# Kernel tuning notes

Measured on AMD Instinct MI355X. Metric: run time of the kernel, lower is better.

The kernel has to match this reference:

```python
import jax, jax.numpy as jnp
import numpy as np

NUM_ITEMS = 100000
OUT_DIM = 128
BATCH = 16384
HIST = 50
TOTAL = BATCH * HIST


def setup_inputs() -> dict:
    key = jax.random.key(0)
    k1, k2, k3, k4, k5, k6 = jax.random.split(key, 6)
    feature_ids = jax.random.randint(k1, (TOTAL,), 0, NUM_ITEMS + 1, dtype=jnp.int64 if jax.config.jax_enable_x64 else jnp.int32)
    # ratings in {0.5, 1.0, ..., 5.0} so that (r - 0.5) * 2 is an int index in [0, 10)
    ratings = jax.random.randint(k2, (TOTAL,), 0, 10).astype(jnp.float32) / 2.0 + 0.5
    segment_ids = jnp.repeat(jnp.arange(BATCH, dtype=jnp.int32), HIST)  # [TOTAL]
    item_ids = jax.random.randint(k3, (BATCH,), 0, NUM_ITEMS, dtype=jnp.int32)
    # kaiming_uniform_(a=sqrt(5)) on an [N, D] table -> U(-b, b) with b = sqrt(6 / ((1 + 5) * D)) = 1/sqrt(D)
    b = 1.0 / np.sqrt(OUT_DIM)
    user_W = jax.random.uniform(k4, (NUM_ITEMS + 1, OUT_DIM), jnp.float32, -b, b)
    rating_W = jax.random.uniform(k5, (10, OUT_DIM), jnp.float32, -b, b)
    item_W = jax.random.uniform(k6, (NUM_ITEMS, OUT_DIM), jnp.float32, -b, b)
    bias = jnp.zeros((OUT_DIM,), jnp.float32)
    return {"feature_ids": feature_ids, "ratings": ratings, "segment_ids": segment_ids,
            "item_ids": item_ids, "user_W": user_W, "rating_W": rating_W,
            "item_W": item_W, "bias": bias}


def reference(feature_ids, ratings, segment_ids, item_ids, user_W, rating_W, item_W, bias):
    batch = item_ids.shape[0]
    rating_idx = ((ratings - 0.5) * 2.0).astype(jnp.int32)          # [T], in [0, 10)
    rating_weights = rating_W[rating_idx]                            # [T, D] gather
    user_weights = user_W[feature_ids] * rating_weights              # [T, D] gather + multiply
    user_sum = jax.ops.segment_sum(user_weights, segment_ids, num_segments=batch)  # [B, D]
    return user_sum + item_W[item_ids] + bias                        # [B, D]
```

## Files before the change

### kernel.cpp

```cpp
#include <hip/hip_runtime.h>


#define BATCH     16384
#define HIST      50
#define TOTAL     (BATCH * HIST)
#define UNROLL    10
#define DIM4      32
#define NROWS_U   100001
#define SLICES    4
#define SL_U4     (NROWS_U * 4)
#define UT_BYTES  ((size_t)SLICES * SL_U4 * 16)
#define RPB       64
#define BLOCK     256
#define RWPAD     36

typedef unsigned int u32x4 __attribute__((ext_vector_type(4)));

__global__ __launch_bounds__(256) void convert_pack_kernel(
    const float4* __restrict__ src,
    const int*    __restrict__ feature_ids,
    const float*  __restrict__ ratings,
    u32x4*        __restrict__ uT,
    int*          __restrict__ packed)
{
    const int tid = blockIdx.x * 256 + threadIdx.x;
    const int stride = gridDim.x * 256;
    if (blockIdx.y < SLICES) {
        const int slice = blockIdx.y;
        u32x4* dst = uT + (size_t)slice * SL_U4;
        for (int i = tid; i < SL_U4; i += stride) {
            const int row = i >> 2, q = i & 3;
            const float4 a = src[row * DIM4 + slice * 8 + q * 2];
            const float4 b = src[row * DIM4 + slice * 8 + q * 2 + 1];
            union { u32x4 v; _Float16 h[8]; } o;
            o.h[0] = (_Float16)a.x; o.h[1] = (_Float16)a.y;
            o.h[2] = (_Float16)a.z; o.h[3] = (_Float16)a.w;
            o.h[4] = (_Float16)b.x; o.h[5] = (_Float16)b.y;
            o.h[6] = (_Float16)b.z; o.h[7] = (_Float16)b.w;
            dst[i] = o.v;
        }
    } else {
        for (int t = tid; t < TOTAL; t += stride) {
            const int fid  = feature_ids[t];
            const int ridx = (int)(ratings[t] * 2.0f) - 1;
            packed[t] = (fid << 4) | ridx;
        }
    }
}

__global__ __launch_bounds__(BLOCK, 4) void features_linear_sliced(
    const int*    __restrict__ packed,
    const int*    __restrict__ item_ids,
    const u32x4*  __restrict__ uT,
    const float*  __restrict__ rating_Wf,
    const float4* __restrict__ item_W,
    const float4* __restrict__ bias,
    float4*       __restrict__ out)
{
    __shared__ int   sh_pid[RPB * HIST];
    __shared__ float sh_rW[10 * RWPAD];

    const int tid   = threadIdx.x;
    const int slice = blockIdx.x & 3;
    const int grp   = blockIdx.x >> 2;

    for (int i = tid; i < 10 * 32; i += BLOCK) {
        const int r = i >> 5, j = i & 31;
        sh_rW[r * RWPAD + j] = rating_Wf[r * 128 + slice * 32 + j];
    }

    const int base = grp * (RPB * HIST);
    for (int i = tid; i < RPB * HIST; i += BLOCK)
        sh_pid[i] = packed[base + i];
    __syncthreads();

    const int row = tid >> 2;
    const int q   = tid & 3;
    const int b   = grp * RPB + row;
    const int off = row * HIST;

    const u32x4* us = uT + (size_t)slice * SL_U4;

    float a0 = 0.f, a1 = 0.f, a2 = 0.f, a3 = 0.f,
          a4 = 0.f, a5 = 0.f, a6 = 0.f, a7 = 0.f;

    for (int h = 0; h < HIST; h += UNROLL) {
        const int p0 = sh_pid[off + h + 0], p1 = sh_pid[off + h + 1];
        const int p2 = sh_pid[off + h + 2], p3 = sh_pid[off + h + 3];
        const int p4 = sh_pid[off + h + 4], p5 = sh_pid[off + h + 5];
        const int p6 = sh_pid[off + h + 6], p7 = sh_pid[off + h + 7];
        const int p8 = sh_pid[off + h + 8], p9 = sh_pid[off + h + 9];

        u32x4 u0 = us[(p0 >> 4) * 4 + q];
        u32x4 u1 = us[(p1 >> 4) * 4 + q];
        u32x4 u2 = us[(p2 >> 4) * 4 + q];
        u32x4 u3 = us[(p3 >> 4) * 4 + q];
        u32x4 u4 = us[(p4 >> 4) * 4 + q];
        u32x4 u5 = us[(p5 >> 4) * 4 + q];
        u32x4 u6 = us[(p6 >> 4) * 4 + q];
        u32x4 u7 = us[(p7 >> 4) * 4 + q];
        u32x4 u8 = us[(p8 >> 4) * 4 + q];
        u32x4 u9 = us[(p9 >> 4) * 4 + q];

        asm volatile("" : "+v"(u0), "+v"(u1), "+v"(u2), "+v"(u3), "+v"(u4),
                          "+v"(u5), "+v"(u6), "+v"(u7), "+v"(u8), "+v"(u9));

#define CONSUME(uk, pk)                                                  \
        {                                                                \
            union { u32x4 v; _Float16 hh[8]; } c; c.v = uk;              \
            const float* w = &sh_rW[(pk & 15) * RWPAD + q * 8];          \
            a0 += (float)c.hh[0] * w[0]; a1 += (float)c.hh[1] * w[1];    \
            a2 += (float)c.hh[2] * w[2]; a3 += (float)c.hh[3] * w[3];    \
            a4 += (float)c.hh[4] * w[4]; a5 += (float)c.hh[5] * w[5];    \
            a6 += (float)c.hh[6] * w[6]; a7 += (float)c.hh[7] * w[7];    \
        }
        CONSUME(u0, p0) CONSUME(u1, p1) CONSUME(u2, p2) CONSUME(u3, p3)
        CONSUME(u4, p4) CONSUME(u5, p5) CONSUME(u6, p6) CONSUME(u7, p7)
        CONSUME(u8, p8) CONSUME(u9, p9)
#undef CONSUME
    }

    const int    iid = item_ids[b];
    const int    e   = slice * 8 + q * 2;
    const float4 iw0 = item_W[iid * DIM4 + e];
    const float4 iw1 = item_W[iid * DIM4 + e + 1];
    const float4 bs0 = bias[e];
    const float4 bs1 = bias[e + 1];

    float4 o0, o1;
    o0.x = a0 + iw0.x + bs0.x; o0.y = a1 + iw0.y + bs0.y;
    o0.z = a2 + iw0.z + bs0.z; o0.w = a3 + iw0.w + bs0.w;
    o1.x = a4 + iw1.x + bs1.x; o1.y = a5 + iw1.y + bs1.y;
    o1.z = a6 + iw1.z + bs1.z; o1.w = a7 + iw1.w + bs1.w;
    out[b * DIM4 + e]     = o0;
    out[b * DIM4 + e + 1] = o1;
}

__global__ __launch_bounds__(BLOCK) void features_linear_f32(
    const int*    __restrict__ feature_ids,
    const float*  __restrict__ ratings,
    const int*    __restrict__ item_ids,
    const float4* __restrict__ user_W,
    const float4* __restrict__ rating_W,
    const float4* __restrict__ item_W,
    const float4* __restrict__ bias,
    float4*       __restrict__ out)
{
    __shared__ float4 sh_rW[10 * DIM4];
    __shared__ int    sh_fid[8 * HIST];
    __shared__ int    sh_ridx[8 * HIST];

    const int tid = threadIdx.x;
    for (int i = tid; i < 10 * DIM4; i += BLOCK) sh_rW[i] = rating_W[i];
    const int base = blockIdx.x * (8 * HIST);
    for (int i = tid; i < 8 * HIST; i += BLOCK) {
        sh_fid[i] = feature_ids[base + i];
        float r = ratings[base + i];
        sh_ridx[i] = (int)(r * 2.0f) - 1;
    }
    __syncthreads();

    const int row = tid >> 5;
    const int d4  = tid & 31;
    const int b   = blockIdx.x * 8 + row;

    float4 acc; acc.x = 0.f; acc.y = 0.f; acc.z = 0.f; acc.w = 0.f;
    const int off = row * HIST;

    for (int h = 0; h < HIST; h += UNROLL) {
        int f[UNROLL], r[UNROLL];
#pragma unroll
        for (int i = 0; i < UNROLL; ++i) {
            f[i] = sh_fid[off + h + i];
            r[i] = sh_ridx[off + h + i];
        }
        float4 u[UNROLL];
#pragma unroll
        for (int i = 0; i < UNROLL; ++i) u[i] = user_W[f[i] * DIM4 + d4];
#pragma unroll
        for (int i = 0; i < UNROLL; ++i) {
            const float4 w = sh_rW[r[i] * DIM4 + d4];
            acc.x += u[i].x * w.x;
            acc.y += u[i].y * w.y;
            acc.z += u[i].z * w.z;
            acc.w += u[i].w * w.w;
        }
    }

    const int    iid = item_ids[b];
    const float4 iw  = item_W[iid * DIM4 + d4];
    const float4 bs  = bias[d4];

    float4 o;
    o.x = acc.x + iw.x + bs.x;
    o.y = acc.y + iw.y + bs.y;
    o.z = acc.z + iw.z + bs.z;
    o.w = acc.w + iw.w + bs.w;
    out[b * DIM4 + d4] = o;
}

extern "C" void kernel_launch(void* const* d_in, const int* in_sizes, int n_in,
                              void* d_out, int out_size, void* d_ws, size_t ws_size,
                              hipStream_t stream) {
    const int*    feature_ids = (const int*)   d_in[0];
    const float*  ratings     = (const float*) d_in[1];
    const int*    item_ids    = (const int*)   d_in[3];
    const float4* user_W      = (const float4*)d_in[4];
    const float4* rating_W    = (const float4*)d_in[5];
    const float4* item_W      = (const float4*)d_in[6];
    const float4* bias        = (const float4*)d_in[7];
    float4*       out         = (float4*)      d_out;

    const size_t need = UT_BYTES + (size_t)TOTAL * sizeof(int);
    if (d_ws != nullptr && ws_size >= need) {
        u32x4* uT     = (u32x4*)d_ws;
        int*   packed = (int*)((char*)d_ws + UT_BYTES);

        convert_pack_kernel<<<dim3(784, 5), dim3(256), 0, stream>>>(
            user_W, feature_ids, ratings, uT, packed);

        features_linear_sliced<<<dim3((BATCH / RPB) * SLICES), dim3(BLOCK), 0, stream>>>(
            packed, item_ids, uT, (const float*)rating_W, item_W, bias, out);
    } else {
        features_linear_f32<<<dim3(BATCH / 8), dim3(BLOCK), 0, stream>>>(
            feature_ids, ratings, item_ids, user_W, rating_W, item_W, bias, out);
    }
}
```

Measured before the change: 167.9 us.

## Split history across half-blocks with shared reduction and coalesce table conversion

The sliced gather kernel now handles 32 rows per block, with two groups of 64 threads each summing half of the 50-entry history for the same rows. The partial sums are then combined through shared memory, and launch bounds are raised to allow 8 blocks per SM for more memory-level parallelism. The fp16 conversion kernel now reads the source table linearly, scatters into the sliced layout, and uses a different grid shape. The cost is an extra barrier and reduction, a lower unroll depth per thread, and scattered writes during conversion.

```diff
diff --git a/kernel.cpp b/kernel.cpp
--- a/kernel.cpp
+++ b/kernel.cpp
@@ -4,13 +4,13 @@
 #define BATCH     16384
 #define HIST      50
 #define TOTAL     (BATCH * HIST)
-#define UNROLL    10
+#define UNROLL    5
 #define DIM4      32
 #define NROWS_U   100001
 #define SLICES    4
 #define SL_U4     (NROWS_U * 4)
 #define UT_BYTES  ((size_t)SLICES * SL_U4 * 16)
-#define RPB       64
+#define RPB       32
 #define BLOCK     256
 #define RWPAD     36
 
@@ -25,19 +25,17 @@
 {
     const int tid = blockIdx.x * 256 + threadIdx.x;
     const int stride = gridDim.x * 256;
-    if (blockIdx.y < SLICES) {
-        const int slice = blockIdx.y;
-        u32x4* dst = uT + (size_t)slice * SL_U4;
-        for (int i = tid; i < SL_U4; i += stride) {
-            const int row = i >> 2, q = i & 3;
-            const float4 a = src[row * DIM4 + slice * 8 + q * 2];
-            const float4 b = src[row * DIM4 + slice * 8 + q * 2 + 1];
+    if (blockIdx.y == 0) {
+        for (int n = tid; n < NROWS_U * 16; n += stride) {
+            const int row = n >> 4, s = (n >> 2) & 3, q = n & 3;
+            const float4 a = src[2 * n];
+            const float4 b = src[2 * n + 1];
             union { u32x4 v; _Float16 h[8]; } o;
             o.h[0] = (_Float16)a.x; o.h[1] = (_Float16)a.y;
             o.h[2] = (_Float16)a.z; o.h[3] = (_Float16)a.w;
             o.h[4] = (_Float16)b.x; o.h[5] = (_Float16)b.y;
             o.h[6] = (_Float16)b.z; o.h[7] = (_Float16)b.w;
-            dst[i] = o.v;
+            uT[(size_t)s * SL_U4 + row * 4 + q] = o.v;
         }
     } else {
         for (int t = tid; t < TOTAL; t += stride) {
@@ -48,7 +46,7 @@
     }
 }
 
-__global__ __launch_bounds__(BLOCK, 4) void features_linear_sliced(
+__global__ __launch_bounds__(BLOCK, 8) void features_linear_sliced(
     const int*    __restrict__ packed,
     const int*    __restrict__ item_ids,
     const u32x4*  __restrict__ uT,
@@ -59,6 +57,7 @@
 {
     __shared__ int   sh_pid[RPB * HIST];
     __shared__ float sh_rW[10 * RWPAD];
+    __shared__ float sh_red[128][8];
 
     const int tid   = threadIdx.x;
     const int slice = blockIdx.x & 3;
@@ -68,72 +67,76 @@
         const int r = i >> 5, j = i & 31;
         sh_rW[r * RWPAD + j] = rating_Wf[r * 128 + slice * 32 + j];
     }
-
     const int base = grp * (RPB * HIST);
     for (int i = tid; i < RPB * HIST; i += BLOCK)
         sh_pid[i] = packed[base + i];
     __syncthreads();
 
-    const int row = tid >> 2;
-    const int q   = tid & 3;
-    const int b   = grp * RPB + row;
-    const int off = row * HIST;
+    const int quad = tid >> 2;
+    const int q    = tid & 3;
+    const int row  = quad & 31;
+    const int hh   = quad >> 5;
+    const int off  = row * HIST + hh * 25;
 
     const u32x4* us = uT + (size_t)slice * SL_U4;
 
     float a0 = 0.f, a1 = 0.f, a2 = 0.f, a3 = 0.f,
           a4 = 0.f, a5 = 0.f, a6 = 0.f, a7 = 0.f;
 
-    for (int h = 0; h < HIST; h += UNROLL) {
+    for (int h = 0; h < 25; h += UNROLL) {
         const int p0 = sh_pid[off + h + 0], p1 = sh_pid[off + h + 1];
         const int p2 = sh_pid[off + h + 2], p3 = sh_pid[off + h + 3];
-        const int p4 = sh_pid[off + h + 4], p5 = sh_pid[off + h + 5];
-        const int p6 = sh_pid[off + h + 6], p7 = sh_pid[off + h + 7];
-        const int p8 = sh_pid[off + h + 8], p9 = sh_pid[off + h + 9];
+        const int p4 = sh_pid[off + h + 4];
 
         u32x4 u0 = us[(p0 >> 4) * 4 + q];
         u32x4 u1 = us[(p1 >> 4) * 4 + q];
         u32x4 u2 = us[(p2 >> 4) * 4 + q];
         u32x4 u3 = us[(p3 >> 4) * 4 + q];
         u32x4 u4 = us[(p4 >> 4) * 4 + q];
-        u32x4 u5 = us[(p5 >> 4) * 4 + q];
-        u32x4 u6 = us[(p6 >> 4) * 4 + q];
-        u32x4 u7 = us[(p7 >> 4) * 4 + q];
-        u32x4 u8 = us[(p8 >> 4) * 4 + q];
-        u32x4 u9 = us[(p9 >> 4) * 4 + q];
-
-        asm volatile("" : "+v"(u0), "+v"(u1), "+v"(u2), "+v"(u3), "+v"(u4),
-                          "+v"(u5), "+v"(u6), "+v"(u7), "+v"(u8), "+v"(u9));
+
+        asm volatile("" : "+v"(u0), "+v"(u1), "+v"(u2), "+v"(u3), "+v"(u4));
 
 #define CONSUME(uk, pk)                                                  \
         {                                                                \
-            union { u32x4 v; _Float16 hh[8]; } c; c.v = uk;              \
+            union { u32x4 v; _Float16 hh_[8]; } c; c.v = uk;             \
             const float* w = &sh_rW[(pk & 15) * RWPAD + q * 8];          \
-            a0 += (float)c.hh[0] * w[0]; a1 += (float)c.hh[1] * w[1];    \
-            a2 += (float)c.hh[2] * w[2]; a3 += (float)c.hh[3] * w[3];    \
-            a4 += (float)c.hh[4] * w[4]; a5 += (float)c.hh[5] * w[5];    \
-            a6 += (float)c.hh[6] * w[6]; a7 += (float)c.hh[7] * w[7];    \
-        }
-        CONSUME(u0, p0) CONSUME(u1, p1) CONSUME(u2, p2) CONSUME(u3, p3)
-        CONSUME(u4, p4) CONSUME(u5, p5) CONSUME(u6, p6) CONSUME(u7, p7)
-        CONSUME(u8, p8) CONSUME(u9, p9)
+            a0 += (float)c.hh_[0] * w[0]; a1 += (float)c.hh_[1] * w[1];  \
+            a2 += (float)c.hh_[2] * w[2]; a3 += (float)c.hh_[3] * w[3];  \
+            a4 += (float)c.hh_[4] * w[4]; a5 += (float)c.hh_[5] * w[5];  \
+            a6 += (float)c.hh_[6] * w[6]; a7 += (float)c.hh_[7] * w[7];  \
+        }
+        CONSUME(u0, p0) CONSUME(u1, p1) CONSUME(u2, p2)
+        CONSUME(u3, p3) CONSUME(u4, p4)
 #undef CONSUME
     }
 
-    const int    iid = item_ids[b];
-    const int    e   = slice * 8 + q * 2;
-    const float4 iw0 = item_W[iid * DIM4 + e];
-    const float4 iw1 = item_W[iid * DIM4 + e + 1];
-    const float4 bs0 = bias[e];
-    const float4 bs1 = bias[e + 1];
-
-    float4 o0, o1;
-    o0.x = a0 + iw0.x + bs0.x; o0.y = a1 + iw0.y + bs0.y;
-    o0.z = a2 + iw0.z + bs0.z; o0.w = a3 + iw0.w + bs0.w;
-    o1.x = a4 + iw1.x + bs1.x; o1.y = a5 + iw1.y + bs1.y;
-    o1.z = a6 + iw1.z + bs1.z; o1.w = a7 + iw1.w + bs1.w;
-    out[b * DIM4 + e]     = o0;
-    out[b * DIM4 + e + 1] = o1;
+    if (hh == 1) {
+        float* d = &sh_red[row * 4 + q][0];
+        d[0] = a0; d[1] = a1; d[2] = a2; d[3] = a3;
+        d[4] = a4; d[5] = a5; d[6] = a6; d[7] = a7;
+    }
+    __syncthreads();
+    if (hh == 0) {
+        const float* p = &sh_red[row * 4 + q][0];
+        a0 += p[0]; a1 += p[1]; a2 += p[2]; a3 += p[3];
+        a4 += p[4]; a5 += p[5]; a6 += p[6]; a7 += p[7];
+
+        const int    b   = grp * RPB + row;
+        const int    iid = item_ids[b];
+        const int    e   = slice * 8 + q * 2;
+        const float4 iw0 = item_W[iid * DIM4 + e];
+        const float4 iw1 = item_W[iid * DIM4 + e + 1];
+        const float4 bs0 = bias[e];
+        const float4 bs1 = bias[e + 1];
+
+        float4 o0, o1;
+        o0.x = a0 + iw0.x + bs0.x; o0.y = a1 + iw0.y + bs0.y;
+        o0.z = a2 + iw0.z + bs0.z; o0.w = a3 + iw0.w + bs0.w;
+        o1.x = a4 + iw1.x + bs1.x; o1.y = a5 + iw1.y + bs1.y;
+        o1.z = a6 + iw1.z + bs1.z; o1.w = a7 + iw1.w + bs1.w;
+        out[b * DIM4 + e]     = o0;
+        out[b * DIM4 + e + 1] = o1;
+    }
 }
 
 __global__ __launch_bounds__(BLOCK) void features_linear_f32(
@@ -167,18 +170,18 @@
     float4 acc; acc.x = 0.f; acc.y = 0.f; acc.z = 0.f; acc.w = 0.f;
     const int off = row * HIST;
 
-    for (int h = 0; h < HIST; h += UNROLL) {
-        int f[UNROLL], r[UNROLL];
+    for (int h = 0; h < HIST; h += 10) {
+        int f[10], r[10];
 #pragma unroll
-        for (int i = 0; i < UNROLL; ++i) {
+        for (int i = 0; i < 10; ++i) {
             f[i] = sh_fid[off + h + i];
             r[i] = sh_ridx[off + h + i];
         }
-        float4 u[UNROLL];
+        float4 u[10];
 #pragma unroll
-        for (int i = 0; i < UNROLL; ++i) u[i] = user_W[f[i] * DIM4 + d4];
+        for (int i = 0; i < 10; ++i) u[i] = user_W[f[i] * DIM4 + d4];
 #pragma unroll
-        for (int i = 0; i < UNROLL; ++i) {
+        for (int i = 0; i < 10; ++i) {
             const float4 w = sh_rW[r[i] * DIM4 + d4];
             acc.x += u[i].x * w.x;
             acc.y += u[i].y * w.y;
@@ -216,7 +219,7 @@
         u32x4* uT     = (u32x4*)d_ws;
         int*   packed = (int*)((char*)d_ws + UT_BYTES);
 
-        convert_pack_kernel<<<dim3(784, 5), dim3(256), 0, stream>>>(
+        convert_pack_kernel<<<dim3(2048, 2), dim3(256), 0, stream>>>(
             user_W, feature_ids, ratings, uT, packed);
 
         features_linear_sliced<<<dim3((BATCH / RPB) * SLICES), dim3(BLOCK), 0, stream>>>(
```

Result: no change. 164.9 us (-1.8%).
